# Kernel tuning notes

Measured on AMD Instinct MI355X. Metric: run time of the kernel, lower is better.

Reference implementation:

```python
import jax, jax.numpy as jnp
import numpy as np

S = 4096          # seq_len (longformer-large-4096)
H = 1024          # hidden_size
FF = 3072         # ffnn_size (hardcoded)
G = 100           # number of gold mentions
MAX_SPAN = 30     # max_span_length
TOP_LAMBDA = 0.2
LN_EPS = 1e-5
MASK_VAL = 10000.0


def setup_inputs() -> dict:
    key = jax.random.key(0)
    ks = jax.random.split(key, 16)
    sc = 0.02
    sequence_output = jax.random.normal(ks[0], (1, S, H), jnp.float32)
    attention_mask = jnp.ones((1, S), jnp.int32)
    # valid gold spans: 1 <= start <= end < start + MAX_SPAN (so torch's >0 filter keeps all)
    gs = jax.random.randint(ks[1], (G,), 1, S - MAX_SPAN)
    gl = jax.random.randint(ks[2], (G,), 0, MAX_SPAN)
    gold_mentions = jnp.stack([gs, gs + gl], axis=1).astype(jnp.int32)  # [G, 2]
    inp = {
        'sequence_output': sequence_output,
        'attention_mask': attention_mask,
        'gold_mentions': gold_mentions,
        # start_mention_mlp
        'W_sm': jax.random.normal(ks[3], (H, FF), jnp.float32) * sc,
        'b_sm': jnp.zeros((FF,), jnp.float32),
        'g_sm': jnp.ones((FF,), jnp.float32),
        'beta_sm': jnp.zeros((FF,), jnp.float32),
        # end_mention_mlp
        'W_em': jax.random.normal(ks[4], (H, FF), jnp.float32) * sc,
        'b_em': jnp.zeros((FF,), jnp.float32),
        'g_em': jnp.ones((FF,), jnp.float32),
        'beta_em': jnp.zeros((FF,), jnp.float32),
        # classifiers
        'w_start': jax.random.normal(ks[5], (FF,), jnp.float32) * sc,
        'b_start': jnp.zeros((), jnp.float32),
        'w_end': jax.random.normal(ks[6], (FF,), jnp.float32) * sc,
        'b_end': jnp.zeros((), jnp.float32),
        'W_s2e': jax.random.normal(ks[7], (FF, FF), jnp.float32) * sc,
        'b_s2e': jnp.zeros((FF,), jnp.float32),
    }
    return inp


def _fcl(x, W, b, g, beta):
    # dense -> gelu (exact) -> layernorm (dropout is identity in eval)
    h = jax.nn.gelu(x @ W + b, approximate=False)
    mu = jnp.mean(h, axis=-1, keepdims=True)
    var = jnp.mean(jnp.square(h - mu), axis=-1, keepdims=True)
    return (h - mu) * jax.lax.rsqrt(var + LN_EPS) * g + beta


def _forward(sequence_output, attention_mask, gold_mentions,
             W_sm, b_sm, g_sm, beta_sm, W_em, b_em, g_em, beta_em,
             w_start, b_start, w_end, b_end, W_s2e, b_s2e):
    start_reps = _fcl(sequence_output, W_sm, b_sm, g_sm, beta_sm)  # [1,S,FF]
    end_reps = _fcl(sequence_output, W_em, b_em, g_em, beta_em)    # [1,S,FF]

    start_logits = jnp.einsum('bsf,f->bs', start_reps, w_start) + b_start  # [1,S]
    end_logits = jnp.einsum('bsf,f->bs', end_reps, w_end) + b_end          # [1,S]
    temp = start_reps @ W_s2e + b_s2e                                      # [1,S,FF]
    joint = jnp.einsum('bsf,btf->bst', temp, end_reps)                     # [1,S,S]
    mention_logits = joint + start_logits[:, :, None] + end_logits[:, None, :]

    # span mask: start <= end < start + MAX_SPAN (triu(0) then tril(MAX_SPAN-1))
    i = jnp.arange(S)
    mention_mask = ((i[:, None] <= i[None, :]) & (i[None, :] < i[:, None] + MAX_SPAN)
                    ).astype(jnp.float32)[None]  # [1,S,S]
    mention_logits = jnp.clip(mention_logits + (1.0 - mention_mask) * (-MASK_VAL),
                              -MASK_VAL, MASK_VAL)

    # top-k pruning; attention_mask is full so k is static: int(S * 0.2)
    max_k = int(S * TOP_LAMBDA)  # 819
    _, topk_1d = jax.lax.top_k(mention_logits.reshape(1, -1), max_k)  # [1,max_k]
    sorted_idx = jnp.sort(topk_1d, axis=-1)
    topk_start_ids = sorted_idx // S
    topk_end_ids = sorted_idx % S
    span_mask = jnp.ones((1, max_k), jnp.float32)

    # losses
    probs = jax.nn.sigmoid(mention_logits)  # [1,S,S]
    gstart = gold_mentions[:, 0]
    gend = gold_mentions[:, 1]
    gold_probs = probs[0, gstart, gend]
    # torch BCE clamps log at -100
    cost_gold = -jnp.mean(jnp.maximum(jnp.log(gold_probs), -100.0))
    junk = probs.at[0, gstart, gend].set(0.0)
    log1mp = jnp.maximum(jnp.log(1.0 - junk), -100.0)
    cost_junk = -jnp.sum(jnp.where(mention_mask == 1.0, log1mp, 0.0)) / jnp.sum(mention_mask)
    cost_is_mention = (cost_gold + cost_junk)[None]  # [1]

    return topk_start_ids, topk_end_ids, span_mask, sequence_output, cost_is_mention


def reference(sequence_output, attention_mask, gold_mentions,
              W_sm, b_sm, g_sm, beta_sm, W_em, b_em, g_em, beta_em,
              w_start, b_start, w_end, b_end, W_s2e, b_s2e):
    return _forward(sequence_output, attention_mask, gold_mentions,
                    W_sm, b_sm, g_sm, beta_sm, W_em, b_em, g_em, beta_em,
                    w_start, b_start, w_end, b_end, W_s2e, b_s2e)
```

## Files before the change

kernel.cpp:

```cpp
#include <hip/hip_runtime.h>
#include <math.h>

#define S 4096
#define H 1024
#define FF 3072
#define G 100
#define MAXSPAN 30
#define MAXK 819
#define NBAND (S * MAXSPAN)
#define BAND_COUNT 122445.0

#define O_START 0
#define O_END   819
#define O_MASK  1638
#define O_SEQ   2457
#define O_COST  (2457 + S * H)

typedef __bf16 bf16x8 __attribute__((ext_vector_type(8)));
typedef float f32x16 __attribute__((ext_vector_type(16)));


__device__ __forceinline__ float block_reduce_256(float x, volatile float* red) {
  #pragma unroll
  for (int off = 32; off > 0; off >>= 1) x += __shfl_down(x, off, 64);
  int wid = threadIdx.x >> 6;
  int lane = threadIdx.x & 63;
  __syncthreads();
  if (lane == 0) red[wid] = x;
  __syncthreads();
  return red[0] + red[1] + red[2] + red[3];
}

__device__ __forceinline__ float block_reduce_1024(float x, volatile float* red) {
  #pragma unroll
  for (int off = 32; off > 0; off >>= 1) x += __shfl_down(x, off, 64);
  int wid = threadIdx.x >> 6;
  int lane = threadIdx.x & 63;
  __syncthreads();
  if (lane == 0) red[wid] = x;
  __syncthreads();
  float s = 0.f;
  #pragma unroll
  for (int q = 0; q < 16; q++) s += red[q];
  return s;
}

__device__ __forceinline__ unsigned f2key(float f) {
  unsigned b = __float_as_uint(f);
  return (b & 0x80000000u) ? ~b : (b | 0x80000000u);
}

__device__ __forceinline__ unsigned short bf16_rne(float x) {
  unsigned u = __float_as_uint(x);
  unsigned r = ((u >> 16) & 1u) + 0x7FFFu;
  return (unsigned short)((u + r) >> 16);
}

__device__ __forceinline__ void split2(float x, unsigned short& h, unsigned short& l) {
  h = bf16_rne(x);
  float hf = __uint_as_float(((unsigned)h) << 16);
  l = bf16_rne(x - hf);
}

__device__ __forceinline__ void gld16(const void* g, void* l) {
  __builtin_amdgcn_global_load_lds(
      (const __attribute__((address_space(1))) unsigned int*)g,
      (__attribute__((address_space(3))) unsigned int*)l, 16, 0, 0);
}


__device__ __forceinline__ void pack_a_body(const float* __restrict__ A,
                                            float* __restrict__ Aout,
                                            unsigned short* __restrict__ hi,
                                            unsigned short* __restrict__ lo,
                                            int K, int bx, int by) {
  __shared__ float tile[32][33];
  const int t = threadIdx.x;
  const int tx = t & 31, ty8 = t >> 5;
  const int k0 = bx * 32, r0 = by * 32;
  #pragma unroll
  for (int r = ty8; r < 32; r += 8) {
    float v = A[(size_t)(r0 + r) * K + k0 + tx];
    tile[r][tx] = v;
    if (Aout) Aout[(size_t)(r0 + r) * K + k0 + tx] = v;
  }
  __syncthreads();
  if (t < 128) {
    const int kql = t >> 5;
    const int rl = t & 31;
    unsigned short h8[8], l8[8];
    #pragma unroll
    for (int s = 0; s < 8; s++) split2(tile[rl][kql * 8 + s], h8[s], l8[s]);
    const size_t panel = (size_t)(r0 >> 7);
    const int rloc = (r0 & 127) + rl;
    const size_t off = panel * (size_t)(128 * K) + (size_t)(k0 / 8 + kql) * 1024 + (size_t)rloc * 8;
    *(uint4*)(hi + off) = *(const uint4*)h8;
    *(uint4*)(lo + off) = *(const uint4*)l8;
  }
}

__device__ __forceinline__ void pack_ln_a_body(const float* __restrict__ A,
                                               const float* __restrict__ mu,
                                               const float* __restrict__ rstd,
                                               const float* __restrict__ g,
                                               const float* __restrict__ beta,
                                               unsigned short* __restrict__ hi,
                                               unsigned short* __restrict__ lo,
                                               int K, int bx, int by) {
  __shared__ float tile[32][33];
  const int t = threadIdx.x;
  const int tx = t & 31, ty8 = t >> 5;
  const int k0 = bx * 32, r0 = by * 32;
  #pragma unroll
  for (int r = ty8; r < 32; r += 8)
    tile[r][tx] = A[(size_t)(r0 + r) * K + k0 + tx];
  __syncthreads();
  if (t < 128) {
    const int kql = t >> 5;
    const int rl = t & 31;
    const int row = r0 + rl;
    const float m = mu[row], rs = rstd[row];
    float4 g0 = *(const float4*)(g + k0 + kql * 8);
    float4 g1 = *(const float4*)(g + k0 + kql * 8 + 4);
    float4 b0 = *(const float4*)(beta + k0 + kql * 8);
    float4 b1 = *(const float4*)(beta + k0 + kql * 8 + 4);
    float gv[8] = {g0.x, g0.y, g0.z, g0.w, g1.x, g1.y, g1.z, g1.w};
    float bv[8] = {b0.x, b0.y, b0.z, b0.w, b1.x, b1.y, b1.z, b1.w};
    unsigned short h8[8], l8[8];
    #pragma unroll
    for (int s = 0; s < 8; s++) {
      float v = (tile[rl][kql * 8 + s] - m) * rs * gv[s] + bv[s];
      split2(v, h8[s], l8[s]);
    }
    const size_t panel = (size_t)(r0 >> 7);
    const int rloc = (r0 & 127) + rl;
    const size_t off = panel * (size_t)(128 * K) + (size_t)(k0 / 8 + kql) * 1024 + (size_t)rloc * 8;
    *(uint4*)(hi + off) = *(const uint4*)h8;
    *(uint4*)(lo + off) = *(const uint4*)l8;
  }
}

__device__ __forceinline__ void pack_bt_body(const float* __restrict__ W,
                                             unsigned short* __restrict__ hi,
                                             unsigned short* __restrict__ lo,
                                             int K, int N, int bx, int by) {
  __shared__ float tile[32][33];
  const int t = threadIdx.x;
  const int tx = t & 31, ty8 = t >> 5;
  const int k0 = bx * 32, n0 = by * 32;
  #pragma unroll
  for (int r = ty8; r < 32; r += 8)
    tile[r][tx] = W[(size_t)(k0 + r) * N + n0 + tx];
  __syncthreads();
  if (t < 128) {
    const int kql = t >> 5;
    const int nl = t & 31;
    unsigned short h8[8], l8[8];
    #pragma unroll
    for (int s = 0; s < 8; s++) split2(tile[kql * 8 + s][nl], h8[s], l8[s]);
    const size_t panel = (size_t)(n0 >> 7);
    const int nloc = (n0 & 127) + nl;
    const size_t off = panel * (size_t)(128 * K) + (size_t)(k0 / 8 + kql) * 1024 + (size_t)nloc * 8;
    *(uint4*)(hi + off) = *(const uint4*)h8;
    *(uint4*)(lo + off) = *(const uint4*)l8;
  }
}

__global__ __launch_bounds__(256) void pack_head_kernel(const float* __restrict__ seq,
                                                        float* __restrict__ seq_out,
                                                        unsigned short* __restrict__ sh,
                                                        unsigned short* __restrict__ sl,
                                                        const float* __restrict__ W1,
                                                        const float* __restrict__ W2,
                                                        unsigned short* __restrict__ w1h,
                                                        unsigned short* __restrict__ w1l,
                                                        unsigned short* __restrict__ w2h,
                                                        unsigned short* __restrict__ w2l) {
  const int y = blockIdx.y;
  if (y < 128)      pack_a_body(seq, seq_out, sh, sl, H, blockIdx.x, y);
  else if (y < 224) pack_bt_body(W1, w1h, w1l, H, FF, blockIdx.x, y - 128);
  else              pack_bt_body(W2, w2h, w2l, H, FF, blockIdx.x, y - 224);
}

__global__ __launch_bounds__(256) void pack_mid_kernel(const float* __restrict__ bufS,
                                                       const float* __restrict__ muS,
                                                       const float* __restrict__ rstdS,
                                                       const float* __restrict__ g,
                                                       const float* __restrict__ beta,
                                                       unsigned short* __restrict__ ahi,
                                                       unsigned short* __restrict__ alo,
                                                       const float* __restrict__ Ws2e,
                                                       unsigned short* __restrict__ wbh,
                                                       unsigned short* __restrict__ wbl) {
  const int y = blockIdx.y;
  if (y < 128) pack_ln_a_body(bufS, muS, rstdS, g, beta, ahi, alo, FF, blockIdx.x, y);
  else         pack_bt_body(Ws2e, wbh, wbl, FF, FF, blockIdx.x, y - 128);
}

#define SLOTB 28672
#define A_STR 8192
#define B_BASE 16384
#define B_STR 6144

template <int EPI>
__device__ __forceinline__ void gemm8_body(const char* __restrict__ cAh, const char* __restrict__ cAl,
                                           const char* __restrict__ cBh, const char* __restrict__ cBl,
                                           const float* __restrict__ bias,
                                           float* __restrict__ C,
                                           int bm, int bn, int N, int K,
                                           char* smem) {
  const int tid = threadIdx.x;
  const int lane = tid & 63;
  const int wid = __builtin_amdgcn_readfirstlane(tid >> 6);
  const int wm = wid >> 1, wn = wid & 1;
  const int khalf = lane >> 5;
  const int r31 = lane & 31;
  const size_t PS = (size_t)256 * (size_t)K;

  const char* lsrc[7];
  int ldst[7];
  #pragma unroll
  for (int i = 0; i < 7; i++) {
    int q = wid * 7 + i;
    if (q < 16) {
      int str = q >> 3, r = q & 7, kql = r >> 2, u = r & 3;
      lsrc[i] = (str ? cAl : cAh) + (size_t)((bm >> 7) + (u >> 1)) * PS
              + (size_t)(kql * 2048 + (u & 1) * 1024 + lane * 16);
      ldst[i] = str * A_STR + kql * 4096 + u * 1024;
    } else {
      int qq = q - 16;
      int str = qq / 6, r = qq % 6, kql = r / 3, v = r % 3;
      int gcol = bn + 64 * v;
      lsrc[i] = (str ? cBl : cBh) + (size_t)(gcol >> 7) * PS
              + (size_t)(kql * 2048 + ((gcol >> 6) & 1) * 1024 + lane * 16);
      ldst[i] = B_BASE + str * B_STR + kql * 3072 + v * 1024;
    }
  }

  const int aoff = khalf * 4096 + (wm * 128 + r31) * 16;
  const int boff = B_BASE + khalf * 3072 + (wn * 96 + r31) * 16;

  f32x16 acc[4][3];
  #pragma unroll
  for (int mt = 0; mt < 4; mt++)
    #pragma unroll
    for (int nt = 0; nt < 3; nt++)
      #pragma unroll
      for (int r = 0; r < 16; r++) acc[mt][nt][r] = 0.0f;

  auto stage = [&](int h) {
    char* sb = smem + (h & 3) * SLOTB;
    const size_t ko = (size_t)h * 4096;
    #pragma unroll
    for (int i = 0; i < 7; i++) gld16(lsrc[i] + ko, sb + ldst[i]);
  };

  const int NH = K >> 4;

  stage(0); stage(1); stage(2);
  asm volatile("s_waitcnt vmcnt(14)" ::: "memory");
  __builtin_amdgcn_s_barrier();

  for (int p = 0; p < NH; ++p) {
    const char* sm = smem + (p & 3) * SLOTB;
    bf16x8 ah[4], al[4], bh[3], bl[3];
    #pragma unroll
    for (int mt = 0; mt < 4; mt++) ah[mt] = *(const bf16x8*)(sm + aoff + mt * 512);
    #pragma unroll
    for (int nt = 0; nt < 3; nt++) bh[nt] = *(const bf16x8*)(sm + boff + nt * 512);
    #pragma unroll
    for (int mt = 0; mt < 4; mt++) al[mt] = *(const bf16x8*)(sm + A_STR + aoff + mt * 512);
    #pragma unroll
    for (int nt = 0; nt < 3; nt++) bl[nt] = *(const bf16x8*)(sm + B_STR + boff + nt * 512);
    if (p + 3 < NH) stage(p + 3);
    __builtin_amdgcn_s_setprio(1);
    #pragma unroll
    for (int mt = 0; mt < 4; mt++)
      #pragma unroll
      for (int nt = 0; nt < 3; nt++) {
        acc[mt][nt] = __builtin_amdgcn_mfma_f32_32x32x16_bf16(ah[mt], bh[nt], acc[mt][nt], 0, 0, 0);
        acc[mt][nt] = __builtin_amdgcn_mfma_f32_32x32x16_bf16(al[mt], bh[nt], acc[mt][nt], 0, 0, 0);
        acc[mt][nt] = __builtin_amdgcn_mfma_f32_32x32x16_bf16(ah[mt], bl[nt], acc[mt][nt], 0, 0, 0);
      }
    __builtin_amdgcn_s_setprio(0);
    if (p + 3 < NH)      { asm volatile("s_waitcnt vmcnt(14)" ::: "memory"); }
    else if (p + 2 < NH) { asm volatile("s_waitcnt vmcnt(7)" ::: "memory"); }
    else if (p + 1 < NH) { asm volatile("s_waitcnt vmcnt(0)" ::: "memory"); }
    if (p + 1 < NH) __builtin_amdgcn_s_barrier();
  }

  #pragma unroll
  for (int mt = 0; mt < 4; mt++) {
    #pragma unroll
    for (int nt = 0; nt < 3; nt++) {
      const int colg = bn + wn * 96 + nt * 32 + r31;
      const float bb = bias[colg];
      #pragma unroll
      for (int reg = 0; reg < 16; reg++) {
        const int rowl = (reg & 3) + 8 * (reg >> 2) + 4 * khalf;
        const int rowg = bm + wm * 128 + mt * 32 + rowl;
        float v = acc[mt][nt][reg] + bb;
        if (EPI == 1) v = 0.5f * v * (1.0f + erff(v * 0.70710678118654752f));
        C[(size_t)rowg * N + colg] = v;
      }
    }
  }
}

__device__ __forceinline__ void grid_swizzle_16x16(int& bx, int& by) {
  const int lin = blockIdx.y * 16 + blockIdx.x;
  const int X = lin & 7, c = lin >> 3;
  bx = (X & 3) * 4 + (c & 3);
  by = (X >> 2) * 8 + (c >> 2);
}

__global__ __launch_bounds__(256, 1) void gemm_mfma_kernel(const unsigned short* __restrict__ Ahi,
                                                           const unsigned short* __restrict__ Alo,
                                                           const unsigned short* __restrict__ Bhi,
                                                           const unsigned short* __restrict__ Blo,
                                                           const float* __restrict__ bias,
                                                           float* __restrict__ C,
                                                           int N, int K) {
  __shared__ __align__(16) char smem[4 * SLOTB];
  int bx, by;
  grid_swizzle_16x16(bx, by);
  gemm8_body<0>((const char*)Ahi, (const char*)Alo,
                (const char*)Bhi, (const char*)Blo,
                bias, C, by * 256, bx * 192, N, K, smem);
}

__global__ __launch_bounds__(256, 1) void gemm_mfma_dual_kernel(const unsigned short* __restrict__ Ahi,
                                                                const unsigned short* __restrict__ Alo,
                                                                const unsigned short* __restrict__ B1hi,
                                                                const unsigned short* __restrict__ B1lo,
                                                                const unsigned short* __restrict__ B2hi,
                                                                const unsigned short* __restrict__ B2lo,
                                                                const float* __restrict__ bias1,
                                                                const float* __restrict__ bias2,
                                                                float* __restrict__ C1,
                                                                float* __restrict__ C2,
                                                                int N, int K) {
  __shared__ __align__(16) char smem[4 * SLOTB];
  const int zb = blockIdx.z;
  const unsigned short* Bhi = zb ? B2hi : B1hi;
  const unsigned short* Blo = zb ? B2lo : B1lo;
  const float* bias = zb ? bias2 : bias1;
  float* C = zb ? C2 : C1;
  int bx, by;
  grid_swizzle_16x16(bx, by);
  gemm8_body<1>((const char*)Ahi, (const char*)Alo,
                (const char*)Bhi, (const char*)Blo,
                bias, C, by * 256, bx * 192, N, K, smem);
}


__global__ __launch_bounds__(256) void ln_stats_kernel(const float* __restrict__ HbS,
                                                       const float* __restrict__ HbE,
                                                       const float* __restrict__ gS,
                                                       const float* __restrict__ betaS,
                                                       const float* __restrict__ wS,
                                                       const float* __restrict__ bS,
                                                       const float* __restrict__ gE,
                                                       const float* __restrict__ betaE,
                                                       const float* __restrict__ wE,
                                                       const float* __restrict__ bE,
                                                       float* __restrict__ slog,
                                                       float* __restrict__ elog,
                                                       float* __restrict__ muS,
                                                       float* __restrict__ rstdS,
                                                       float* __restrict__ muE,
                                                       float* __restrict__ rstdE) {
  __shared__ float red[4];
  const int row = blockIdx.x, tid = threadIdx.x;
  const int br = blockIdx.y;
  const float* Hb = br ? HbE : HbS;
  const float* g = br ? gE : gS;
  const float* beta = br ? betaE : betaS;
  const float* w = br ? wE : wS;
  const float* bsc = br ? bE : bS;
  const float* h = Hb + (size_t)row * FF;

  float4 v[3];
  float s = 0.0f;
  #pragma unroll
  for (int t = 0; t < 3; t++) {
    v[t] = *(const float4*)(h + tid * 4 + t * 1024);
    s += v[t].x + v[t].y + v[t].z + v[t].w;
  }
  float mu = block_reduce_256(s, red) * (1.0f / (float)FF);

  float s2 = 0.0f;
  #pragma unroll
  for (int t = 0; t < 3; t++) {
    float dx = v[t].x - mu, dy = v[t].y - mu, dz = v[t].z - mu, dw = v[t].w - mu;
    s2 += dx * dx + dy * dy + dz * dz + dw * dw;
  }
  float var = block_reduce_256(s2, red) * (1.0f / (float)FF);
  float rstd = rsqrtf(var + 1e-5f);

  float dot = 0.0f;
  #pragma unroll
  for (int t = 0; t < 3; t++) {
    int idx = tid * 4 + t * 1024;
    float4 gv = *(const float4*)(g + idx);
    float4 bv = *(const float4*)(beta + idx);
    float4 wv = *(const float4*)(w + idx);
    float rx = (v[t].x - mu) * rstd * gv.x + bv.x;
    float ry = (v[t].y - mu) * rstd * gv.y + bv.y;
    float rz = (v[t].z - mu) * rstd * gv.z + bv.z;
    float rw = (v[t].w - mu) * rstd * gv.w + bv.w;
    dot += rx * wv.x + ry * wv.y + rz * wv.z + rw * wv.w;
  }
  float dt = block_reduce_256(dot, red);
  if (tid == 0) {
    if (br) { elog[row] = dt + bsc[0]; muE[row] = mu; rstdE[row] = rstd; }
    else    { slog[row] = dt + bsc[0]; muS[row] = mu; rstdS[row] = rstd; }
  }
}


__global__ __launch_bounds__(256) void band_joint_kernel(const float* __restrict__ T,
                                                         const float* __restrict__ Eraw,
                                                         const float* __restrict__ muE,
                                                         const float* __restrict__ rstdE,
                                                         const float* __restrict__ gE,
                                                         const float* __restrict__ betaE,
                                                         const float* __restrict__ sl,
                                                         const float* __restrict__ el,
                                                         float* __restrict__ band,
                                                         double* __restrict__ jacc,
                                                         unsigned* __restrict__ hist16) {
  __shared__ float Elds[45][260];
  __shared__ float red[4];
  const int t = threadIdx.x;
  const int bx = blockIdx.x;
  const int sbx = (bx & 7) * 32 + (bx >> 3);
  const int i0 = sbx * 16;
  const int r_l = t >> 4, c = t & 15;

  float accd[MAXSPAN];
  #pragma unroll
  for (int d = 0; d < MAXSPAN; d++) accd[d] = 0.0f;

  for (int k0 = 0; k0 < FF; k0 += 256) {
    const float* trow = T + (size_t)(i0 + r_l) * FF + k0 + c * 16;
    float4 tv0 = *(const float4*)(trow + 0);
    float4 tv1 = *(const float4*)(trow + 4);
    float4 tv2 = *(const float4*)(trow + 8);
    float4 tv3 = *(const float4*)(trow + 12);
    __syncthreads();
    for (int rr = t >> 6; rr < 45; rr += 4) {
      int gr = i0 + rr;
      int cc = (t & 63) * 4;
      float4 rv = {0.f, 0.f, 0.f, 0.f};
      if (gr < S) {
        float4 ev = *(const float4*)(Eraw + (size_t)gr * FF + k0 + cc);
        float m = muE[gr], rs = rstdE[gr];
        float4 gv = *(const float4*)(gE + k0 + cc);
        float4 bv = *(const float4*)(betaE + k0 + cc);
        rv.x = (ev.x - m) * rs * gv.x + bv.x;
        rv.y = (ev.y - m) * rs * gv.y + bv.y;
        rv.z = (ev.z - m) * rs * gv.z + bv.z;
        rv.w = (ev.w - m) * rs * gv.w + bv.w;
      }
      *(float4*)&Elds[rr][cc] = rv;
    }
    __syncthreads();
    #pragma unroll
    for (int d = 0; d < MAXSPAN; d++) {
      const float* er = &Elds[r_l + d][c * 16];
      float4 e0 = *(const float4*)(er + 0);
      float4 e1 = *(const float4*)(er + 4);
      float4 e2 = *(const float4*)(er + 8);
      float4 e3 = *(const float4*)(er + 12);
      accd[d] += tv0.x * e0.x + tv0.y * e0.y + tv0.z * e0.z + tv0.w * e0.w
               + tv1.x * e1.x + tv1.y * e1.y + tv1.z * e1.z + tv1.w * e1.w
               + tv2.x * e2.x + tv2.y * e2.y + tv2.z * e2.z + tv2.w * e2.w
               + tv3.x * e3.x + tv3.y * e3.y + tv3.z * e3.z + tv3.w * e3.w;
    }
  }

  const int i = i0 + r_l;
  const float my_sl = sl[i];
  float jsum = 0.0f;
  #pragma unroll
  for (int d = 0; d < MAXSPAN; d++) {
    float v = accd[d];
    v += __shfl_down(v, 8, 16);
    v += __shfl_down(v, 4, 16);
    v += __shfl_down(v, 2, 16);
    v += __shfl_down(v, 1, 16);
    if (c == 0) {
      int j = i + d;
      if (j < S) {
        float vv = v + my_sl + el[j];
        vv = fminf(fmaxf(vv, -10000.0f), 10000.0f);
        band[i * MAXSPAN + d] = vv;
        atomicAdd(&hist16[f2key(vv) >> 16], 1u);
        float p = 1.0f / (1.0f + expf(-vv));
        jsum += fmaxf(logf(1.0f - p), -100.0f);
      } else {
        band[i * MAXSPAN + d] = -1e30f;
      }
    }
  }
  float tot = block_reduce_256(jsum, red);
  if (t == 0) atomicAdd(jacc, (double)tot);
}


__global__ __launch_bounds__(1024) void topk_finalize_kernel(const float* __restrict__ band,
                                                             const int* __restrict__ gold,
                                                             const double* __restrict__ jacc,
                                                             const unsigned* __restrict__ hist16,
                                                             float* __restrict__ out) {
  __shared__ int csum[1024];
  __shared__ unsigned sh_T16;
  __shared__ int sh_remk;
  __shared__ int sh_chunk, sh_above;
  __shared__ int idxbuf[1024];
  __shared__ unsigned tkey[256];
  __shared__ int tidx[256];
  __shared__ int cnt_gt, cnt_eq;
  __shared__ int sb[1024];
  __shared__ int gcell[G];
  __shared__ float redf[16];
  const int tid = threadIdx.x;

  int s = 0;
  #pragma unroll 8
  for (int q = 0; q < 64; q++) s += (int)hist16[tid * 64 + q];
  csum[tid] = s;
  __syncthreads();
  for (int off = 1; off < 1024; off <<= 1) {
    int v = (tid + off < 1024) ? csum[tid + off] : 0;
    __syncthreads();
    csum[tid] += v;
    __syncthreads();
  }
  {
    int nxt = (tid < 1023) ? csum[tid + 1] : 0;
    if (csum[tid] >= MAXK && nxt < MAXK) { sh_chunk = tid; sh_above = nxt; }
  }
  __syncthreads();
  if (tid == 0) {
    int cum = sh_above;
    int b = sh_chunk * 64 + 63;
    for (;; b--) {
      int h = (int)hist16[b];
      if (cum + h >= MAXK || b == sh_chunk * 64) { sh_T16 = (unsigned)b; sh_remk = MAXK - cum; break; }
      cum += h;
    }
  }
  __syncthreads();
  const unsigned T16 = sh_T16;
  int remk = sh_remk;

  if (tid == 0) { cnt_gt = 0; cnt_eq = 0; }
  __syncthreads();
  for (int e = tid; e < NBAND; e += 1024) {
    unsigned key = f2key(band[e]);
    unsigned k16 = key >> 16;
    if (k16 >= T16) {
      int i = e / MAXSPAN, d = e - i * MAXSPAN;
      int fi = i * S + i + d;
      if (k16 > T16) {
        int p = atomicAdd(&cnt_gt, 1);
        if (p < 1024) idxbuf[p] = fi;
      } else {
        int p = atomicAdd(&cnt_eq, 1);
        if (p < 256) { tkey[p] = key; tidx[p] = fi; }
      }
    }
  }
  __syncthreads();
  if (tid == 0) {
    int ngt = cnt_gt < 1024 ? cnt_gt : 1024;
    int ne = cnt_eq < 256 ? cnt_eq : 256;
    for (int a2 = 1; a2 < ne; a2++) {
      unsigned kv = tkey[a2]; int iv = tidx[a2];
      int b2 = a2 - 1;
      while (b2 >= 0 && (tkey[b2] < kv || (tkey[b2] == kv && tidx[b2] > iv))) {
        tkey[b2 + 1] = tkey[b2]; tidx[b2 + 1] = tidx[b2]; b2--;
      }
      tkey[b2 + 1] = kv; tidx[b2 + 1] = iv;
    }
    int take = remk < ne ? remk : ne;
    for (int q = 0; q < take; q++)
      if (ngt + q < 1024) idxbuf[ngt + q] = tidx[q];
  }
  __syncthreads();

  sb[tid] = (tid < MAXK) ? idxbuf[tid] : 0x7FFFFFFF;
  __syncthreads();
  for (int ksz = 2; ksz <= 1024; ksz <<= 1) {
    for (int jj = ksz >> 1; jj > 0; jj >>= 1) {
      int ixj = tid ^ jj;
      if (ixj > tid) {
        int a2 = sb[tid], b2 = sb[ixj];
        bool up = ((tid & ksz) == 0);
        if (up ? (a2 > b2) : (a2 < b2)) { sb[tid] = b2; sb[ixj] = a2; }
      }
      __syncthreads();
    }
  }
  if (tid < MAXK) {
    int fi = sb[tid];
    out[O_START + tid] = (float)(fi >> 12);
    out[O_END + tid]   = (float)(fi & 4095);
    out[O_MASK + tid]  = 1.0f;
  }

  if (tid < G) {
    int gs = gold[2 * tid], ge = gold[2 * tid + 1];
    gcell[tid] = gs * MAXSPAN + (ge - gs);
  }
  __syncthreads();
  float tg = 0.0f, tj = 0.0f;
  if (tid < G) {
    int cell = gcell[tid];
    float x = band[cell];
    float p = 1.0f / (1.0f + expf(-x));
    tg = fmaxf(logf(p), -100.0f);
    bool first = true;
    for (int q = 0; q < tid; q++)
      if (gcell[q] == cell) { first = false; break; }
    if (first) tj = fmaxf(logf(1.0f - p), -100.0f);
  }
  float sg = block_reduce_1024(tg, redf);
  float sj = block_reduce_1024(tj, redf);
  if (tid == 0) {
    double junk = *jacc - (double)sj;
    double cost = -((double)sg / (double)G) - (junk / BAND_COUNT);
    out[O_COST] = (float)cost;
  }
}


extern "C" void kernel_launch(void* const* d_in, const int* in_sizes, int n_in,
                              void* d_out, int out_size, void* d_ws, size_t ws_size,
                              hipStream_t stream) {
  (void)in_sizes; (void)n_in; (void)out_size; (void)ws_size;
  const float* seq    = (const float*)d_in[0];
  const int*   gold   = (const int*)d_in[2];
  const float* W_sm   = (const float*)d_in[3];
  const float* b_sm   = (const float*)d_in[4];
  const float* g_sm   = (const float*)d_in[5];
  const float* be_sm  = (const float*)d_in[6];
  const float* W_em   = (const float*)d_in[7];
  const float* b_em   = (const float*)d_in[8];
  const float* g_em   = (const float*)d_in[9];
  const float* be_em  = (const float*)d_in[10];
  const float* w_st   = (const float*)d_in[11];
  const float* b_st   = (const float*)d_in[12];
  const float* w_en   = (const float*)d_in[13];
  const float* b_en   = (const float*)d_in[14];
  const float* W_s2e  = (const float*)d_in[15];
  const float* b_s2e  = (const float*)d_in[16];
  float* out = (float*)d_out;
  char* ws = (char*)d_ws;

  const size_t SZ_REP = (size_t)S * FF * 4;
  float*  bufS = (float*)(ws);
  float*  bufE = (float*)(ws + SZ_REP);
  float*  bufT = (float*)(ws + 2 * SZ_REP);
  char* R3 = ws + 3 * SZ_REP;
  unsigned short* seqhi = (unsigned short*)R3;
  unsigned short* seqlo = (unsigned short*)(R3 + (size_t)S * H * 2);
  unsigned short* a3hi  = (unsigned short*)R3;
  unsigned short* a3lo  = (unsigned short*)(R3 + (size_t)S * FF * 2);
  char* R4 = ws + 4 * SZ_REP;
  const size_t SZ_W12 = (size_t)H * FF * 2;
  unsigned short* wb1hi = (unsigned short*)R4;
  unsigned short* wb1lo = (unsigned short*)(R4 + SZ_W12);
  unsigned short* wb2hi = (unsigned short*)(R4 + 2 * SZ_W12);
  unsigned short* wb2lo = (unsigned short*)(R4 + 3 * SZ_W12);
  unsigned short* wbhi = (unsigned short*)R4;
  unsigned short* wblo = (unsigned short*)(R4 + (size_t)FF * FF * 2);
  char* R5 = R4 + 2 * (size_t)FF * FF * 2;
  float*    band   = (float*)R5;
  unsigned* hist16 = (unsigned*)(R5 + (size_t)NBAND * 4);
  double*   jacc   = (double*)(R5 + (size_t)NBAND * 4 + 262144);
  float*    slog   = (float*)(R5 + (size_t)NBAND * 4 + 262144 + 64);
  float*  elog  = slog + S;
  float*  muS   = elog + S;
  float*  rstdS = muS + S;
  float*  muE   = rstdS + S;
  float*  rstdE = muE + S;

  hipMemsetAsync(hist16, 0, 262144 + 64 + 8, stream);

  dim3 gg(16, 16);
  dim3 gg2(16, 16, 2);

  pack_head_kernel<<<dim3(32, 320), 256, 0, stream>>>(seq, out + O_SEQ, seqhi, seqlo,
                                                      W_sm, W_em, wb1hi, wb1lo, wb2hi, wb2lo);
  gemm_mfma_dual_kernel<<<gg2, 256, 0, stream>>>(seqhi, seqlo, wb1hi, wb1lo, wb2hi, wb2lo,
                                                 b_sm, b_em, bufS, bufE, FF, H);
  ln_stats_kernel<<<dim3(S, 2), 256, 0, stream>>>(bufS, bufE, g_sm, be_sm, w_st, b_st,
                                                  g_em, be_em, w_en, b_en,
                                                  slog, elog, muS, rstdS, muE, rstdE);
  pack_mid_kernel<<<dim3(96, 224), 256, 0, stream>>>(bufS, muS, rstdS, g_sm, be_sm,
                                                     a3hi, a3lo, W_s2e, wbhi, wblo);
  gemm_mfma_kernel<<<gg, 256, 0, stream>>>(a3hi, a3lo, wbhi, wblo, b_s2e, bufT, FF, FF);

  band_joint_kernel<<<S / 16, 256, 0, stream>>>(bufT, bufE, muE, rstdE, g_em, be_em,
                                                slog, elog, band, jacc, hist16);

  topk_finalize_kernel<<<1, 1024, 0, stream>>>(band, gold, jacc, hist16, out);
}
```

Measured before the change: 811.2 us.

## Fuse LN-normalized A packing into ln_stats and parallelize top-k tie sort

The layer-normalised start activations are now split into hi/lo bf16 and written in the packed GEMM layout directly inside ln_stats_kernel. That removes the second pass in pack_mid_kernel that re-read the 4096x3072 fp32 buffer, so pack_mid now only packs W_s2e. In the top-k finalize kernel, the single-thread insertion sort of tied keys becomes a 256-wide bitonic sort, the histogram sum uses vector loads, and the threshold scan reads the 64 bins from shared memory. The risk is that the bitonic sort pads with sentinel values and must reproduce the original ordering of tied entries.

```diff
diff --git a/kernel.cpp b/kernel.cpp
--- a/kernel.cpp
+++ b/kernel.cpp
@@ -91,47 +91,6 @@
     unsigned short h8[8], l8[8];
     #pragma unroll
     for (int s = 0; s < 8; s++) split2(tile[rl][kql * 8 + s], h8[s], l8[s]);
-    const size_t panel = (size_t)(r0 >> 7);
-    const int rloc = (r0 & 127) + rl;
-    const size_t off = panel * (size_t)(128 * K) + (size_t)(k0 / 8 + kql) * 1024 + (size_t)rloc * 8;
-    *(uint4*)(hi + off) = *(const uint4*)h8;
-    *(uint4*)(lo + off) = *(const uint4*)l8;
-  }
-}
-
-__device__ __forceinline__ void pack_ln_a_body(const float* __restrict__ A,
-                                               const float* __restrict__ mu,
-                                               const float* __restrict__ rstd,
-                                               const float* __restrict__ g,
-                                               const float* __restrict__ beta,
-                                               unsigned short* __restrict__ hi,
-                                               unsigned short* __restrict__ lo,
-                                               int K, int bx, int by) {
-  __shared__ float tile[32][33];
-  const int t = threadIdx.x;
-  const int tx = t & 31, ty8 = t >> 5;
-  const int k0 = bx * 32, r0 = by * 32;
-  #pragma unroll
-  for (int r = ty8; r < 32; r += 8)
-    tile[r][tx] = A[(size_t)(r0 + r) * K + k0 + tx];
-  __syncthreads();
-  if (t < 128) {
-    const int kql = t >> 5;
-    const int rl = t & 31;
-    const int row = r0 + rl;
-    const float m = mu[row], rs = rstd[row];
-    float4 g0 = *(const float4*)(g + k0 + kql * 8);
-    float4 g1 = *(const float4*)(g + k0 + kql * 8 + 4);
-    float4 b0 = *(const float4*)(beta + k0 + kql * 8);
-    float4 b1 = *(const float4*)(beta + k0 + kql * 8 + 4);
-    float gv[8] = {g0.x, g0.y, g0.z, g0.w, g1.x, g1.y, g1.z, g1.w};
-    float bv[8] = {b0.x, b0.y, b0.z, b0.w, b1.x, b1.y, b1.z, b1.w};
-    unsigned short h8[8], l8[8];
-    #pragma unroll
-    for (int s = 0; s < 8; s++) {
-      float v = (tile[rl][kql * 8 + s] - m) * rs * gv[s] + bv[s];
-      split2(v, h8[s], l8[s]);
-    }
     const size_t panel = (size_t)(r0 >> 7);
     const int rloc = (r0 & 127) + rl;
     const size_t off = panel * (size_t)(128 * K) + (size_t)(k0 / 8 + kql) * 1024 + (size_t)rloc * 8;
@@ -182,19 +141,10 @@
   else              pack_bt_body(W2, w2h, w2l, H, FF, blockIdx.x, y - 224);
 }
 
-__global__ __launch_bounds__(256) void pack_mid_kernel(const float* __restrict__ bufS,
-                                                       const float* __restrict__ muS,
-                                                       const float* __restrict__ rstdS,
-                                                       const float* __restrict__ g,
-                                                       const float* __restrict__ beta,
-                                                       unsigned short* __restrict__ ahi,
-                                                       unsigned short* __restrict__ alo,
-                                                       const float* __restrict__ Ws2e,
+__global__ __launch_bounds__(256) void pack_mid_kernel(const float* __restrict__ Ws2e,
                                                        unsigned short* __restrict__ wbh,
                                                        unsigned short* __restrict__ wbl) {
-  const int y = blockIdx.y;
-  if (y < 128) pack_ln_a_body(bufS, muS, rstdS, g, beta, ahi, alo, FF, blockIdx.x, y);
-  else         pack_bt_body(Ws2e, wbh, wbl, FF, FF, blockIdx.x, y - 128);
+  pack_bt_body(Ws2e, wbh, wbl, FF, FF, blockIdx.x, blockIdx.y);
 }
 
 #define SLOTB 28672
@@ -369,7 +319,9 @@
                                                        float* __restrict__ muS,
                                                        float* __restrict__ rstdS,
                                                        float* __restrict__ muE,
-                                                       float* __restrict__ rstdE) {
+                                                       float* __restrict__ rstdE,
+                                                       unsigned short* __restrict__ a3hi,
+                                                       unsigned short* __restrict__ a3lo) {
   __shared__ float red[4];
   const int row = blockIdx.x, tid = threadIdx.x;
   const int br = blockIdx.y;
@@ -398,6 +350,7 @@
   float var = block_reduce_256(s2, red) * (1.0f / (float)FF);
   float rstd = rsqrtf(var + 1e-5f);
 
+  float4 nv[3];
   float dot = 0.0f;
   #pragma unroll
   for (int t = 0; t < 3; t++) {
@@ -409,12 +362,35 @@
     float ry = (v[t].y - mu) * rstd * gv.y + bv.y;
     float rz = (v[t].z - mu) * rstd * gv.z + bv.z;
     float rw = (v[t].w - mu) * rstd * gv.w + bv.w;
+    nv[t] = make_float4(rx, ry, rz, rw);
     dot += rx * wv.x + ry * wv.y + rz * wv.z + rw * wv.w;
   }
   float dt = block_reduce_256(dot, red);
   if (tid == 0) {
     if (br) { elog[row] = dt + bsc[0]; muE[row] = mu; rstdE[row] = rstd; }
     else    { slog[row] = dt + bsc[0]; muS[row] = mu; rstdS[row] = rstd; }
+  }
+
+  if (br == 0) {
+    const size_t panel = (size_t)(row >> 7);
+    const int rloc = row & 127;
+    #pragma unroll
+    for (int t = 0; t < 3; t++) {
+      float o0 = __shfl_xor(nv[t].x, 1, 64);
+      float o1 = __shfl_xor(nv[t].y, 1, 64);
+      float o2 = __shfl_xor(nv[t].z, 1, 64);
+      float o3 = __shfl_xor(nv[t].w, 1, 64);
+      if ((tid & 1) == 0) {
+        float f8[8] = {nv[t].x, nv[t].y, nv[t].z, nv[t].w, o0, o1, o2, o3};
+        unsigned short h8[8], l8[8];
+        #pragma unroll
+        for (int q = 0; q < 8; q++) split2(f8[q], h8[q], l8[q]);
+        const int kq = t * 128 + (tid >> 1);
+        const size_t off = panel * (size_t)(128 * FF) + (size_t)kq * 1024 + (size_t)rloc * 8;
+        *(uint4*)(a3hi + off) = *(const uint4*)h8;
+        *(uint4*)(a3lo + off) = *(const uint4*)l8;
+      }
+    }
   }
 }
 
@@ -518,6 +494,7 @@
   __shared__ unsigned sh_T16;
   __shared__ int sh_remk;
   __shared__ int sh_chunk, sh_above;
+  __shared__ unsigned hbin[64];
   __shared__ int idxbuf[1024];
   __shared__ unsigned tkey[256];
   __shared__ int tidx[256];
@@ -528,9 +505,16 @@
   const int tid = threadIdx.x;
 
   int s = 0;
-  #pragma unroll 8
-  for (int q = 0; q < 64; q++) s += (int)hist16[tid * 64 + q];
+  {
+    const uint4* hv = (const uint4*)hist16 + (size_t)tid * 16;
+    #pragma unroll
+    for (int q = 0; q < 16; q++) {
+      uint4 u = hv[q];
+      s += (int)(u.x + u.y + u.z + u.w);
+    }
+  }
   csum[tid] = s;
+  if (tid < 256) { tkey[tid] = 0u; tidx[tid] = 0x7FFFFFFF; }
   __syncthreads();
   for (int off = 1; off < 1024; off <<= 1) {
     int v = (tid + off < 1024) ? csum[tid + off] : 0;
@@ -543,12 +527,14 @@
     if (csum[tid] >= MAXK && nxt < MAXK) { sh_chunk = tid; sh_above = nxt; }
   }
   __syncthreads();
+  if (tid < 64) hbin[tid] = hist16[sh_chunk * 64 + tid];
+  __syncthreads();
   if (tid == 0) {
     int cum = sh_above;
-    int b = sh_chunk * 64 + 63;
+    int b = 63;
     for (;; b--) {
-      int h = (int)hist16[b];
-      if (cum + h >= MAXK || b == sh_chunk * 64) { sh_T16 = (unsigned)b; sh_remk = MAXK - cum; break; }
+      int h = (int)hbin[b];
+      if (cum + h >= MAXK || b == 0) { sh_T16 = (unsigned)(sh_chunk * 64 + b); sh_remk = MAXK - cum; break; }
       cum += h;
     }
   }
@@ -574,20 +560,30 @@
     }
   }
   __syncthreads();
-  if (tid == 0) {
+
+  for (int ksz2 = 2; ksz2 <= 256; ksz2 <<= 1) {
+    for (int jj = ksz2 >> 1; jj > 0; jj >>= 1) {
+      if (tid < 256) {
+        int ixj = tid ^ jj;
+        if (ixj > tid) {
+          unsigned ka = tkey[tid], kb = tkey[ixj];
+          int ia = tidx[tid], ib = tidx[ixj];
+          bool aFirst = (ka > kb) || (ka == kb && ia < ib);
+          bool up = ((tid & ksz2) == 0);
+          if (up ? !aFirst : aFirst) {
+            tkey[tid] = kb; tidx[tid] = ib;
+            tkey[ixj] = ka; tidx[ixj] = ia;
+          }
+        }
+      }
+      __syncthreads();
+    }
+  }
+  {
     int ngt = cnt_gt < 1024 ? cnt_gt : 1024;
     int ne = cnt_eq < 256 ? cnt_eq : 256;
-    for (int a2 = 1; a2 < ne; a2++) {
-      unsigned kv = tkey[a2]; int iv = tidx[a2];
-      int b2 = a2 - 1;
-      while (b2 >= 0 && (tkey[b2] < kv || (tkey[b2] == kv && tidx[b2] > iv))) {
-        tkey[b2 + 1] = tkey[b2]; tidx[b2 + 1] = tidx[b2]; b2--;
-      }
-      tkey[b2 + 1] = kv; tidx[b2 + 1] = iv;
-    }
     int take = remk < ne ? remk : ne;
-    for (int q = 0; q < take; q++)
-      if (ngt + q < 1024) idxbuf[ngt + q] = tidx[q];
+    if (tid < take && ngt + tid < 1024) idxbuf[ngt + tid] = tidx[tid];
   }
   __syncthreads();
 
@@ -699,9 +695,9 @@
                                                  b_sm, b_em, bufS, bufE, FF, H);
   ln_stats_kernel<<<dim3(S, 2), 256, 0, stream>>>(bufS, bufE, g_sm, be_sm, w_st, b_st,
                                                   g_em, be_em, w_en, b_en,
-                                                  slog, elog, muS, rstdS, muE, rstdE);
-  pack_mid_kernel<<<dim3(96, 224), 256, 0, stream>>>(bufS, muS, rstdS, g_sm, be_sm,
-                                                     a3hi, a3lo, W_s2e, wbhi, wblo);
+                                                  slog, elog, muS, rstdS, muE, rstdE,
+                                                  a3hi, a3lo);
+  pack_mid_kernel<<<dim3(96, 96), 256, 0, stream>>>(W_s2e, wbhi, wblo);
   gemm_mfma_kernel<<<gg, 256, 0, stream>>>(a3hi, a3lo, wbhi, wblo, b_s2e, bufT, FF, FF);
 
   band_joint_kernel<<<S / 16, 256, 0, stream>>>(bufT, bufE, muE, rstdE, g_em, be_em,
```

Result: slower. 984.8 us (+21.4%).
